# Performance work log

Measured on AMD Instinct MI355X. Metric: run time of the kernel, lower is better.

The kernel has to match this reference:

```python
import jax, jax.numpy as jnp
import numpy as np

N = 100000
IN_DIM, HID_DIM, EMB_DIM = 128, 64, 32
E = 1600000


def _gcn_conv(x, W, b, src, tgt, n):
    """PyG GCNConv: linear transform, add self-loops, sym-normalized scatter-add.
    W: [in, out], b: [out]. src/tgt: [E'] incl. self-loops handled by caller."""
    h = x @ W  # [n, out] -- transform before propagate (PyG order)
    deg = jax.ops.segment_sum(jnp.ones_like(tgt, dtype=h.dtype), tgt, num_segments=n)
    dinv = jnp.where(deg > 0, jax.lax.rsqrt(deg), 0.0)
    norm = dinv[src] * dinv[tgt]  # [E']
    msgs = h[src] * norm[:, None]  # [E', out]
    out = jax.ops.segment_sum(msgs, tgt, num_segments=n)
    return out + b


def setup_inputs() -> dict:
    key = jax.random.key(0)
    ks = jax.random.split(key, 6)
    x = jax.random.normal(ks[0], (N, IN_DIM), dtype=jnp.float32)
    edge_index = jax.random.randint(ks[1], (2, E), 0, N, dtype=jnp.int64)
    s1 = 1.0 / np.sqrt(IN_DIM)
    s2 = 1.0 / np.sqrt(HID_DIM)
    W1 = jax.random.uniform(ks[2], (IN_DIM, HID_DIM), jnp.float32, -s1, s1)
    b1 = jnp.zeros((HID_DIM,), jnp.float32)
    W2 = jax.random.uniform(ks[3], (HID_DIM, EMB_DIM), jnp.float32, -s2, s2)
    b2 = jnp.zeros((EMB_DIM,), jnp.float32)
    return {"x": x, "W1": W1, "b1": b1, "W2": W2, "b2": b2, "edge_index": edge_index}


def reference(x, W1, b1, W2, b2, edge_index):
    n = x.shape[0]
    src, tgt = edge_index[0], edge_index[1]
    # add self-loops once (same graph used by both convs)
    loops = jnp.arange(n, dtype=edge_index.dtype)
    src_sl = jnp.concatenate([src, loops])
    tgt_sl = jnp.concatenate([tgt, loops])
    h = jax.nn.relu(_gcn_conv(x, W1, b1, src_sl, tgt_sl, n))
    z = _gcn_conv(h, W2, b2, src_sl, tgt_sl, n)  # [n, EMB_DIM]
    # decode on original edges: edge-wise dot product
    recon = jnp.sum(z[src] * z[tgt], axis=1)  # [E]
    return z, recon
```

## Files before the change

kernel.cpp:

```cpp
#include <hip/hip_runtime.h>
#include <hip/hip_fp16.h>
#include <math.h>


#define NBMAX 256
#define BSHIFT 9
#define BNODES 512
#define CH 4096
#define CAPSHIFT 14
#define CAP (1 << CAPSHIFT)

typedef _Float16 half8 __attribute__((ext_vector_type(8)));
typedef float floatx4 __attribute__((ext_vector_type(4)));

static inline int divup(int a, int b) { return (a + b - 1) / b; }

__device__ inline void acc8(__half2* a, float4 v) {
    const __half2* h = (const __half2*)&v;
    a[0] = __hadd2(a[0], h[0]);
    a[1] = __hadd2(a[1], h[1]);
    a[2] = __hadd2(a[2], h[2]);
    a[3] = __hadd2(a[3], h[3]);
}
__device__ inline unsigned short f2bf(float f) {
    unsigned u = __builtin_bit_cast(unsigned, f);
    u = (u + 0x7FFFu + ((u >> 16) & 1u)) >> 16;
    return (unsigned short)u;
}


__global__ void k_init(int* __restrict__ gcur, unsigned* __restrict__ hs_pad,
                       unsigned* __restrict__ zs_pad) {
    int t = threadIdx.x;
    if (t < NBMAX) gcur[t] = t << CAPSHIFT;
    if (t < 32) hs_pad[t] = 0;
    else if (t < 48) zs_pad[t - 32] = 0;
}


__global__ __launch_bounds__(256) void k_part(const int* __restrict__ src,
                                              const int* __restrict__ tgt,
                                              int* __restrict__ gcur,
                                              unsigned* __restrict__ ebuf, int E, int NB) {
    __shared__ int h[NBMAX];
    __shared__ int base[NBMAX];
    int tid = threadIdx.x;
    int e0 = blockIdx.x * CH;
    for (int b = tid; b < NB; b += 256) h[b] = 0;
    __syncthreads();
    unsigned pk[CH / 256];
    int sv[CH / 256];
#pragma unroll
    for (int r = 0; r < CH / 256; r++) {
        int e = e0 + r * 256 + tid;
        if (e < E) {
            int t = tgt[e];
            int b = t >> BSHIFT;
            int l = atomicAdd(&h[b], 1);
            pk[r] = ((unsigned)b << 21) | ((unsigned)(t & (BNODES - 1)) << 12) | (unsigned)l;
            sv[r] = src[e];
        } else {
            pk[r] = 0xFFFFFFFFu;
        }
    }
    __syncthreads();
    for (int b = tid; b < NB; b += 256) {
        int c = h[b];
        base[b] = c ? atomicAdd(&gcur[b], c) : 0;
    }
    __syncthreads();
#pragma unroll
    for (int r = 0; r < CH / 256; r++) {
        if (pk[r] != 0xFFFFFFFFu) {
            int b = pk[r] >> 21;
            unsigned lt = (pk[r] >> 12) & (BNODES - 1);
            int l = pk[r] & 4095;
            ebuf[base[b] + l] = (lt << 23) | (unsigned)sv[r];
        }
    }
}


__global__ __launch_bounds__(512) void k_bfill(const unsigned* __restrict__ ebuf,
                                               const int* __restrict__ gcur,
                                               int* __restrict__ rowbeg,
                                               int* __restrict__ rowend,
                                               int* __restrict__ col,
                                               float* __restrict__ dinv, int n) {
    __shared__ int s_cnt[BNODES];
    __shared__ int s_scan[BNODES];
    __shared__ int s_cur[BNODES];
    int b = blockIdx.x, tid = threadIdx.x;
    int nbase = b << BSHIFT;
    int ebase = b << CAPSHIFT;
    int eend = gcur[b];
    s_cnt[tid] = 0;
    __syncthreads();
    for (int e = ebase + tid; e < eend; e += BNODES) {
        atomicAdd(&s_cnt[ebuf[e] >> 23], 1);
    }
    __syncthreads();
    s_scan[tid] = s_cnt[tid];
    __syncthreads();
    for (int off = 1; off < BNODES; off <<= 1) {
        int t = (tid >= off) ? s_scan[tid - off] : 0;
        __syncthreads();
        s_scan[tid] += t;
        __syncthreads();
    }
    int excl = s_scan[tid] - s_cnt[tid];
    s_cur[tid] = excl;
    int node = nbase + tid;
    if (node < n) {
        rowbeg[node] = ebase + excl;
        rowend[node] = ebase + excl + s_cnt[tid];
        dinv[node] = rsqrtf((float)(s_cnt[tid] + 1));
    }
    __syncthreads();
    for (int e = ebase + tid; e < eend; e += BNODES) {
        unsigned p = ebuf[e];
        int pos = atomicAdd(&s_cur[p >> 23], 1);
        col[ebase + pos] = (int)(p & 0x7FFFFFu);
    }
}


__global__ __launch_bounds__(256) void k_mm1(const float* __restrict__ x,
                                             const float* __restrict__ W1,
                                             const float* __restrict__ dinv,
                                             __half* __restrict__ hs, int n) {
    __shared__ _Float16 xh[64 * 136];
    __shared__ _Float16 Wt[64 * 136];
    int tid = threadIdx.x;
    int nbase = blockIdx.x * 64;
#pragma unroll
    for (int i = 0; i < 8; i++) {
        int f = tid + i * 256;
        int r = f >> 5, c4 = f & 31;
        int node = nbase + r;
        float4 v = make_float4(0.f, 0.f, 0.f, 0.f);
        if (node < n) v = *(const float4*)(x + (size_t)node * 128 + c4 * 4);
        union { uint2 u; __half2 h[2]; } pk;
        pk.h[0] = __floats2half2_rn(v.x, v.y);
        pk.h[1] = __floats2half2_rn(v.z, v.w);
        *(uint2*)&xh[r * 136 + c4 * 4] = pk.u;
    }
#pragma unroll
    for (int i = 0; i < 16; i++) {
        int f = tid + i * 256;
        int c = f & 63, kp = f >> 6;
        float a = W1[(size_t)(2 * kp) * 64 + c];
        float b = W1[(size_t)(2 * kp + 1) * 64 + c];
        *(__half2*)&Wt[c * 136 + 2 * kp] = __floats2half2_rn(a, b);
    }
    __syncthreads();
    int w = tid >> 6, lane = tid & 63;
    int quad = lane >> 4, m = lane & 15;
    floatx4 acc[4] = {{0.f, 0.f, 0.f, 0.f}, {0.f, 0.f, 0.f, 0.f},
                      {0.f, 0.f, 0.f, 0.f}, {0.f, 0.f, 0.f, 0.f}};
#pragma unroll
    for (int kt = 0; kt < 4; kt++) {
        half8 a = *(const half8*)&xh[(w * 16 + m) * 136 + kt * 32 + quad * 8];
#pragma unroll
        for (int ct = 0; ct < 4; ct++) {
            half8 b = *(const half8*)&Wt[(ct * 16 + m) * 136 + kt * 32 + quad * 8];
            acc[ct] = __builtin_amdgcn_mfma_f32_16x16x32_f16(a, b, acc[ct], 0, 0, 0);
        }
    }
#pragma unroll
    for (int reg = 0; reg < 4; reg++) {
        int node = nbase + w * 16 + quad * 4 + reg;
        if (node < n) {
            float d = dinv[node];
#pragma unroll
            for (int ct = 0; ct < 4; ct++) {
                hs[(size_t)node * 64 + ct * 16 + m] = __float2half(acc[ct][reg] * d);
            }
        }
    }
}


__global__ __launch_bounds__(256) void k_conv1(const __half* __restrict__ hs,
                                               const int* __restrict__ rowbeg,
                                               const int* __restrict__ rowend,
                                               const int* __restrict__ col,
                                               const float* __restrict__ dinv,
                                               const float* __restrict__ b1,
                                               __half* __restrict__ h2, int n) {
    int w = (blockIdx.x * 256 + threadIdx.x) >> 6;
    int lane = threadIdx.x & 63;
    if (w >= n) return;
    int el = lane >> 3, fl = lane & 7;
    int beg = rowbeg[w], end = rowend[w];
    int deg = end - beg;
    int m = min(64, deg);
    int sl = (lane < m) ? col[beg + lane] : 0;
    int s0 = __shfl(sl, el);
    int s1 = __shfl(sl, 8 + el);
    int s2 = __shfl(sl, 16 + el);
    int s3 = __shfl(sl, 24 + el);
    int r0 = (el < m) ? s0 : n;
    int r1 = (8 + el < m) ? s1 : n;
    int r2 = (16 + el < m) ? s2 : n;
    int r3 = (24 + el < m) ? s3 : n;
    int rs = (el == 0) ? w : n;
    float4 S = *(const float4*)(hs + (size_t)rs * 64 + fl * 8);
    float4 A = *(const float4*)(hs + (size_t)r0 * 64 + fl * 8);
    float4 B = *(const float4*)(hs + (size_t)r1 * 64 + fl * 8);
    float4 C = *(const float4*)(hs + (size_t)r2 * 64 + fl * 8);
    float4 D = *(const float4*)(hs + (size_t)r3 * 64 + fl * 8);
    __half2 a2[4];
#pragma unroll
    for (int j = 0; j < 4; j++) a2[j] = __half2half2(__float2half(0.f));
    acc8(a2, S);
    acc8(a2, A);
    acc8(a2, B);
    acc8(a2, C);
    acc8(a2, D);
    if (deg > 32) {
        for (int i = 32; i < m; i += 8) {
            int idx = i + el;
            int s = __shfl(sl, idx & 63);
            int a = (idx < m) ? s : n;
            float4 v = *(const float4*)(hs + (size_t)a * 64 + fl * 8);
            acc8(a2, v);
        }
        for (int e0 = beg + 64; e0 < end; e0 += 64) {
            int mc = min(64, end - e0);
            int sl2 = (lane < mc) ? col[e0 + lane] : 0;
            for (int i = 0; i < mc; i += 8) {
                int idx = i + el;
                int s = __shfl(sl2, idx & 63);
                int a = (idx < mc) ? s : n;
                float4 v = *(const float4*)(hs + (size_t)a * 64 + fl * 8);
                acc8(a2, v);
            }
        }
    }
    float r[8];
#pragma unroll
    for (int j = 0; j < 4; j++) {
        float2 f = __half22float2(a2[j]);
        r[2 * j] = f.x;
        r[2 * j + 1] = f.y;
    }
    for (int d = 8; d < 64; d <<= 1)
#pragma unroll
        for (int j = 0; j < 8; j++) r[j] += __shfl_xor(r[j], d);

    if (el == 0) {
        float d = dinv[w];
        float4 bb0 = *(const float4*)(b1 + fl * 8);
        float4 bb1 = *(const float4*)(b1 + fl * 8 + 4);
        union { float4 f; __half2 h[4]; } u;
        u.h[0] = __floats2half2_rn(fmaxf(r[0] * d + bb0.x, 0.f),
                                   fmaxf(r[1] * d + bb0.y, 0.f));
        u.h[1] = __floats2half2_rn(fmaxf(r[2] * d + bb0.z, 0.f),
                                   fmaxf(r[3] * d + bb0.w, 0.f));
        u.h[2] = __floats2half2_rn(fmaxf(r[4] * d + bb1.x, 0.f),
                                   fmaxf(r[5] * d + bb1.y, 0.f));
        u.h[3] = __floats2half2_rn(fmaxf(r[6] * d + bb1.z, 0.f),
                                   fmaxf(r[7] * d + bb1.w, 0.f));
        *(float4*)(h2 + (size_t)w * 64 + fl * 8) = u.f;
    }
}


__global__ __launch_bounds__(256) void k_mm2(const __half* __restrict__ h2,
                                             const float* __restrict__ W2,
                                             const float* __restrict__ dinv,
                                             __half* __restrict__ zs, int n) {
    __shared__ _Float16 Wt[32 * 72];
    int tid = threadIdx.x;
    int nbase = blockIdx.x * 64;
#pragma unroll
    for (int i = 0; i < 4; i++) {
        int f = tid + i * 256;
        int c = f & 31, kp = f >> 5;
        float a = W2[(size_t)(2 * kp) * 32 + c];
        float b = W2[(size_t)(2 * kp + 1) * 32 + c];
        *(__half2*)&Wt[c * 72 + 2 * kp] = __floats2half2_rn(a, b);
    }
    __syncthreads();
    int w = tid >> 6, lane = tid & 63;
    int quad = lane >> 4, m = lane & 15;
    int arow = nbase + w * 16 + m;
    const __half* abase = h2 + (size_t)min(arow, n - 1) * 64;
    floatx4 acc[2] = {{0.f, 0.f, 0.f, 0.f}, {0.f, 0.f, 0.f, 0.f}};
#pragma unroll
    for (int kt = 0; kt < 2; kt++) {
        half8 a = *(const half8*)(abase + kt * 32 + quad * 8);
#pragma unroll
        for (int ct = 0; ct < 2; ct++) {
            half8 b = *(const half8*)&Wt[(ct * 16 + m) * 72 + kt * 32 + quad * 8];
            acc[ct] = __builtin_amdgcn_mfma_f32_16x16x32_f16(a, b, acc[ct], 0, 0, 0);
        }
    }
#pragma unroll
    for (int reg = 0; reg < 4; reg++) {
        int node = nbase + w * 16 + quad * 4 + reg;
        if (node < n) {
            float d = dinv[node];
#pragma unroll
            for (int ct = 0; ct < 2; ct++) {
                zs[(size_t)node * 32 + ct * 16 + m] = __float2half(acc[ct][reg] * d);
            }
        }
    }
}


__global__ __launch_bounds__(256) void k_conv2(const __half* __restrict__ zs,
                                               const int* __restrict__ rowbeg,
                                               const int* __restrict__ rowend,
                                               const int* __restrict__ col,
                                               const float* __restrict__ dinv,
                                               const float* __restrict__ b2,
                                               float* __restrict__ zout,
                                               unsigned short* __restrict__ zh, int n) {
    int w = (blockIdx.x * 256 + threadIdx.x) >> 6;
    int lane = threadIdx.x & 63;
    if (w >= n) return;
    int el = lane >> 2, fl = lane & 3;
    int beg = rowbeg[w], end = rowend[w];
    int deg = end - beg;
    int m = min(64, deg);
    int sl = (lane < m) ? col[beg + lane] : 0;
    int s0 = __shfl(sl, el);
    int s1 = __shfl(sl, 16 + el);
    int r0 = (el < m) ? s0 : n;
    int r1 = (16 + el < m) ? s1 : n;
    int rs = (el == 0) ? w : n;
    float4 S = *(const float4*)(zs + (size_t)rs * 32 + fl * 8);
    float4 A = *(const float4*)(zs + (size_t)r0 * 32 + fl * 8);
    float4 B = *(const float4*)(zs + (size_t)r1 * 32 + fl * 8);
    __half2 a2[4];
#pragma unroll
    for (int j = 0; j < 4; j++) a2[j] = __half2half2(__float2half(0.f));
    acc8(a2, S);
    acc8(a2, A);
    acc8(a2, B);
    if (deg > 32) {
        int s2 = __shfl(sl, 32 + el);
        int s3 = __shfl(sl, 48 + el);
        int r2 = (32 + el < m) ? s2 : n;
        int r3 = (48 + el < m) ? s3 : n;
        float4 C = *(const float4*)(zs + (size_t)r2 * 32 + fl * 8);
        float4 D = *(const float4*)(zs + (size_t)r3 * 32 + fl * 8);
        acc8(a2, C);
        acc8(a2, D);
        for (int e0 = beg + 64; e0 < end; e0 += 64) {
            int mc = min(64, end - e0);
            int sl2 = (lane < mc) ? col[e0 + lane] : 0;
            for (int i = 0; i < mc; i += 16) {
                int idx = i + el;
                int s = __shfl(sl2, idx & 63);
                int a = (idx < mc) ? s : n;
                float4 v = *(const float4*)(zs + (size_t)a * 32 + fl * 8);
                acc8(a2, v);
            }
        }
    }
    float r[8];
#pragma unroll
    for (int j = 0; j < 4; j++) {
        float2 f = __half22float2(a2[j]);
        r[2 * j] = f.x;
        r[2 * j + 1] = f.y;
    }
    for (int d = 4; d < 64; d <<= 1)
#pragma unroll
        for (int j = 0; j < 8; j++) r[j] += __shfl_xor(r[j], d);

    if (el == 0) {
        float d = dinv[w];
        float4 bb0 = *(const float4*)(b2 + fl * 8);
        float4 bb1 = *(const float4*)(b2 + fl * 8 + 4);
        float o0 = r[0] * d + bb0.x, o1 = r[1] * d + bb0.y;
        float o2 = r[2] * d + bb0.z, o3 = r[3] * d + bb0.w;
        float o4 = r[4] * d + bb1.x, o5 = r[5] * d + bb1.y;
        float o6 = r[6] * d + bb1.z, o7 = r[7] * d + bb1.w;
        *(float4*)(zout + (size_t)w * 32 + fl * 8) = make_float4(o0, o1, o2, o3);
        *(float4*)(zout + (size_t)w * 32 + fl * 8 + 4) = make_float4(o4, o5, o6, o7);
        uint4 p;
        p.x = (unsigned)f2bf(o0) | ((unsigned)f2bf(o1) << 16);
        p.y = (unsigned)f2bf(o2) | ((unsigned)f2bf(o3) << 16);
        p.z = (unsigned)f2bf(o4) | ((unsigned)f2bf(o5) << 16);
        p.w = (unsigned)f2bf(o6) | ((unsigned)f2bf(o7) << 16);
        *(uint4*)(zh + (size_t)w * 32 + fl * 8) = p;
    }
}


__device__ inline float bfdot8(uint4 a, uint4 b) {
    const unsigned* pa = (const unsigned*)&a;
    const unsigned* pb = (const unsigned*)&b;
    float v = 0.f;
#pragma unroll
    for (int w = 0; w < 4; w++) {
        float alo = __builtin_bit_cast(float, pa[w] << 16);
        float ahi = __builtin_bit_cast(float, pa[w] & 0xFFFF0000u);
        float blo = __builtin_bit_cast(float, pb[w] << 16);
        float bhi = __builtin_bit_cast(float, pb[w] & 0xFFFF0000u);
        v += alo * blo + ahi * bhi;
    }
    return v;
}

__global__ __launch_bounds__(256) void k_decode(const unsigned short* __restrict__ zh,
                                                const int* __restrict__ src,
                                                const int* __restrict__ tgt,
                                                float* __restrict__ recon, int E) {
    int g = (blockIdx.x * 256 + threadIdx.x) >> 2;
    int fl = threadIdx.x & 3;
    int e0 = g * 4;
    if (e0 >= E) return;
    int cnt = min(4, E - e0);
    int s[4], t[4];
#pragma unroll
    for (int q = 0; q < 4; q++) {
        int e = (q < cnt) ? e0 + q : e0;
        s[q] = src[e];
        t[q] = tgt[e];
    }
    uint4 Za[4], Zb[4];
#pragma unroll
    for (int q = 0; q < 4; q++) {
        Za[q] = *(const uint4*)(zh + (size_t)s[q] * 32 + fl * 8);
        Zb[q] = *(const uint4*)(zh + (size_t)t[q] * 32 + fl * 8);
    }
    float v[4];
#pragma unroll
    for (int q = 0; q < 4; q++) {
        float x = bfdot8(Za[q], Zb[q]);
        x += __shfl_xor(x, 1);
        x += __shfl_xor(x, 2);
        v[q] = x;
    }
    if (fl == 0) {
        if (cnt == 4) {
            *(float4*)(recon + e0) = make_float4(v[0], v[1], v[2], v[3]);
        } else {
            for (int q = 0; q < cnt; q++) recon[e0 + q] = v[q];
        }
    }
}

extern "C" void kernel_launch(void* const* d_in, const int* in_sizes, int n_in,
                              void* d_out, int out_size, void* d_ws, size_t ws_size,
                              hipStream_t stream) {
    const float* x = (const float*)d_in[0];
    const float* W1 = (const float*)d_in[1];
    const float* b1 = (const float*)d_in[2];
    const float* W2 = (const float*)d_in[3];
    const float* b2 = (const float*)d_in[4];
    const int* ei = (const int*)d_in[5];

    int N = in_sizes[0] / 128;
    int E = in_sizes[5] / 2;
    const int* src = ei;
    const int* tgt = ei + E;
    int NB = divup(N, BNODES);

    char* ws = (char*)d_ws;
    size_t off = 0;
    auto alloc = [&](size_t bytes) {
        size_t r = off;
        off += (bytes + 255) & ~(size_t)255;
        return r;
    };
    int* gcur = (int*)(ws + alloc(NBMAX * 4));
    unsigned* ebuf = (unsigned*)(ws + alloc((size_t)NB * CAP * 4));
    int* col = (int*)(ws + alloc((size_t)NB * CAP * 4));
    int* rowbeg = (int*)(ws + alloc((size_t)N * 4));
    int* rowend = (int*)(ws + alloc((size_t)N * 4));
    float* dinv = (float*)(ws + alloc((size_t)N * 4));
    __half* hs = (__half*)(ws + alloc((size_t)(N + 1) * 64 * 2));
    __half* h2 = (__half*)(ws + alloc((size_t)N * 64 * 2));
    __half* zs = (__half*)(ws + alloc((size_t)(N + 1) * 32 * 2));
    unsigned short* zh = (unsigned short*)(ws + alloc((size_t)N * 32 * 2));

    float* zout = (float*)d_out;
    float* recon = zout + (size_t)N * 32;

    k_init<<<1, 256, 0, stream>>>(gcur, (unsigned*)(hs + (size_t)N * 64),
                                  (unsigned*)(zs + (size_t)N * 32));
    k_part<<<divup(E, CH), 256, 0, stream>>>(src, tgt, gcur, ebuf, E, NB);
    k_bfill<<<NB, BNODES, 0, stream>>>(ebuf, gcur, rowbeg, rowend, col, dinv, N);

    k_mm1<<<divup(N, 64), 256, 0, stream>>>(x, W1, dinv, hs, N);
    k_conv1<<<divup(N, 4), 256, 0, stream>>>(hs, rowbeg, rowend, col, dinv, b1, h2, N);
    k_mm2<<<divup(N, 64), 256, 0, stream>>>(h2, W2, dinv, zs, N);
    k_conv2<<<divup(N, 4), 256, 0, stream>>>(zs, rowbeg, rowend, col, dinv, b2, zout, zh, N);
    k_decode<<<divup(E, 256), 256, 0, stream>>>(zh, src, tgt, recon, E);
}
```

Before: 258.7 us.

## Process two nodes per wavefront in GCN aggregation kernels using half-wave groups

Both conv aggregation kernels now split each 64-lane wavefront into two 32-lane halves, each handling its own target node, and the grid is halved to match. Average in-degree is about 17, so a full wave per node left many lanes idle and paid per-row overhead once per wave; packing two rows per wave is meant to raise lane utilization and cut wave count. In exchange there is more divergence between the halves, whose degrees differ, and the reduction tree is shortened to stay within 32 lanes.

```diff
diff --git a/kernel.cpp b/kernel.cpp
--- a/kernel.cpp
+++ b/kernel.cpp
@@ -188,22 +188,25 @@
                                                const float* __restrict__ dinv,
                                                const float* __restrict__ b1,
                                                __half* __restrict__ h2, int n) {
-    int w = (blockIdx.x * 256 + threadIdx.x) >> 6;
+    int gw = (blockIdx.x * 256 + threadIdx.x) >> 6;
     int lane = threadIdx.x & 63;
+    int half = lane >> 5, ln = lane & 31;
+    int w = gw * 2 + half;
     if (w >= n) return;
-    int el = lane >> 3, fl = lane & 7;
+    int hbase = half << 5;
+    int el = ln >> 3, fl = ln & 7;
     int beg = rowbeg[w], end = rowend[w];
     int deg = end - beg;
-    int m = min(64, deg);
-    int sl = (lane < m) ? col[beg + lane] : 0;
-    int s0 = __shfl(sl, el);
-    int s1 = __shfl(sl, 8 + el);
-    int s2 = __shfl(sl, 16 + el);
-    int s3 = __shfl(sl, 24 + el);
+    int m = min(32, deg);
+    int sl = (ln < m) ? col[beg + ln] : 0;
+    int s0 = __shfl(sl, hbase + el);
+    int s1 = __shfl(sl, hbase + 4 + el);
+    int s2 = __shfl(sl, hbase + 8 + el);
+    int s3 = __shfl(sl, hbase + 12 + el);
     int r0 = (el < m) ? s0 : n;
-    int r1 = (8 + el < m) ? s1 : n;
-    int r2 = (16 + el < m) ? s2 : n;
-    int r3 = (24 + el < m) ? s3 : n;
+    int r1 = (4 + el < m) ? s1 : n;
+    int r2 = (8 + el < m) ? s2 : n;
+    int r3 = (12 + el < m) ? s3 : n;
     int rs = (el == 0) ? w : n;
     float4 S = *(const float4*)(hs + (size_t)rs * 64 + fl * 8);
     float4 A = *(const float4*)(hs + (size_t)r0 * 64 + fl * 8);
@@ -218,20 +221,31 @@
     acc8(a2, B);
     acc8(a2, C);
     acc8(a2, D);
+    if (deg > 16) {
+        int t0 = __shfl(sl, hbase + 16 + el);
+        int t1 = __shfl(sl, hbase + 20 + el);
+        int t2 = __shfl(sl, hbase + 24 + el);
+        int t3 = __shfl(sl, hbase + 28 + el);
+        int q0 = (16 + el < m) ? t0 : n;
+        int q1 = (20 + el < m) ? t1 : n;
+        int q2 = (24 + el < m) ? t2 : n;
+        int q3 = (28 + el < m) ? t3 : n;
+        float4 E0 = *(const float4*)(hs + (size_t)q0 * 64 + fl * 8);
+        float4 E1 = *(const float4*)(hs + (size_t)q1 * 64 + fl * 8);
+        float4 E2 = *(const float4*)(hs + (size_t)q2 * 64 + fl * 8);
+        float4 E3 = *(const float4*)(hs + (size_t)q3 * 64 + fl * 8);
+        acc8(a2, E0);
+        acc8(a2, E1);
+        acc8(a2, E2);
+        acc8(a2, E3);
+    }
     if (deg > 32) {
-        for (int i = 32; i < m; i += 8) {
-            int idx = i + el;
-            int s = __shfl(sl, idx & 63);
-            int a = (idx < m) ? s : n;
-            float4 v = *(const float4*)(hs + (size_t)a * 64 + fl * 8);
-            acc8(a2, v);
-        }
-        for (int e0 = beg + 64; e0 < end; e0 += 64) {
-            int mc = min(64, end - e0);
-            int sl2 = (lane < mc) ? col[e0 + lane] : 0;
-            for (int i = 0; i < mc; i += 8) {
+        for (int b0 = 32; b0 < deg; b0 += 32) {
+            int mc = min(32, deg - b0);
+            int sl2 = (ln < mc) ? col[beg + b0 + ln] : 0;
+            for (int i = 0; i < mc; i += 4) {
                 int idx = i + el;
-                int s = __shfl(sl2, idx & 63);
+                int s = __shfl(sl2, hbase + (idx & 31));
                 int a = (idx < mc) ? s : n;
                 float4 v = *(const float4*)(hs + (size_t)a * 64 + fl * 8);
                 acc8(a2, v);
@@ -245,7 +259,8 @@
         r[2 * j] = f.x;
         r[2 * j + 1] = f.y;
     }
-    for (int d = 8; d < 64; d <<= 1)
+#pragma unroll
+    for (int d = 8; d < 32; d <<= 1)
 #pragma unroll
         for (int j = 0; j < 8; j++) r[j] += __shfl_xor(r[j], d);
 
@@ -319,18 +334,21 @@
                                                const float* __restrict__ b2,
                                                float* __restrict__ zout,
                                                unsigned short* __restrict__ zh, int n) {
-    int w = (blockIdx.x * 256 + threadIdx.x) >> 6;
+    int gw = (blockIdx.x * 256 + threadIdx.x) >> 6;
     int lane = threadIdx.x & 63;
+    int half = lane >> 5, ln = lane & 31;
+    int w = gw * 2 + half;
     if (w >= n) return;
-    int el = lane >> 2, fl = lane & 3;
+    int hbase = half << 5;
+    int el = ln >> 2, fl = ln & 3;
     int beg = rowbeg[w], end = rowend[w];
     int deg = end - beg;
-    int m = min(64, deg);
-    int sl = (lane < m) ? col[beg + lane] : 0;
-    int s0 = __shfl(sl, el);
-    int s1 = __shfl(sl, 16 + el);
+    int m = min(32, deg);
+    int sl = (ln < m) ? col[beg + ln] : 0;
+    int s0 = __shfl(sl, hbase + el);
+    int s1 = __shfl(sl, hbase + 8 + el);
     int r0 = (el < m) ? s0 : n;
-    int r1 = (16 + el < m) ? s1 : n;
+    int r1 = (8 + el < m) ? s1 : n;
     int rs = (el == 0) ? w : n;
     float4 S = *(const float4*)(zs + (size_t)rs * 32 + fl * 8);
     float4 A = *(const float4*)(zs + (size_t)r0 * 32 + fl * 8);
@@ -341,21 +359,23 @@
     acc8(a2, S);
     acc8(a2, A);
     acc8(a2, B);
-    if (deg > 32) {
-        int s2 = __shfl(sl, 32 + el);
-        int s3 = __shfl(sl, 48 + el);
-        int r2 = (32 + el < m) ? s2 : n;
-        int r3 = (48 + el < m) ? s3 : n;
+    if (deg > 16) {
+        int s2 = __shfl(sl, hbase + 16 + el);
+        int s3 = __shfl(sl, hbase + 24 + el);
+        int r2 = (16 + el < m) ? s2 : n;
+        int r3 = (24 + el < m) ? s3 : n;
         float4 C = *(const float4*)(zs + (size_t)r2 * 32 + fl * 8);
         float4 D = *(const float4*)(zs + (size_t)r3 * 32 + fl * 8);
         acc8(a2, C);
         acc8(a2, D);
-        for (int e0 = beg + 64; e0 < end; e0 += 64) {
-            int mc = min(64, end - e0);
-            int sl2 = (lane < mc) ? col[e0 + lane] : 0;
-            for (int i = 0; i < mc; i += 16) {
+    }
+    if (deg > 32) {
+        for (int b0 = 32; b0 < deg; b0 += 32) {
+            int mc = min(32, deg - b0);
+            int sl2 = (ln < mc) ? col[beg + b0 + ln] : 0;
+            for (int i = 0; i < mc; i += 8) {
                 int idx = i + el;
-                int s = __shfl(sl2, idx & 63);
+                int s = __shfl(sl2, hbase + (idx & 31));
                 int a = (idx < mc) ? s : n;
                 float4 v = *(const float4*)(zs + (size_t)a * 32 + fl * 8);
                 acc8(a2, v);
@@ -369,7 +389,8 @@
         r[2 * j] = f.x;
         r[2 * j + 1] = f.y;
     }
-    for (int d = 4; d < 64; d <<= 1)
+#pragma unroll
+    for (int d = 4; d < 32; d <<= 1)
 #pragma unroll
         for (int j = 0; j < 8; j++) r[j] += __shfl_xor(r[j], d);
 
@@ -490,8 +511,8 @@
     k_bfill<<<NB, BNODES, 0, stream>>>(ebuf, gcur, rowbeg, rowend, col, dinv, N);
 
     k_mm1<<<divup(N, 64), 256, 0, stream>>>(x, W1, dinv, hs, N);
-    k_conv1<<<divup(N, 4), 256, 0, stream>>>(hs, rowbeg, rowend, col, dinv, b1, h2, N);
+    k_conv1<<<divup(N, 8), 256, 0, stream>>>(hs, rowbeg, rowend, col, dinv, b1, h2, N);
     k_mm2<<<divup(N, 64), 256, 0, stream>>>(h2, W2, dinv, zs, N);
-    k_conv2<<<divup(N, 4), 256, 0, stream>>>(zs, rowbeg, rowend, col, dinv, b2, zout, zh, N);
+    k_conv2<<<divup(N, 8), 256, 0, stream>>>(zs, rowbeg, rowend, col, dinv, b2, zout, zh, N);
     k_decode<<<divup(E, 256), 256, 0, stream>>>(zh, src, tgt, recon, E);
 }
```

New measurement: 233.8 us. 9.6% less time.

## Map four nodes per wavefront in GCN aggregation and vectorize edge partition loads

Applied to the files above, without the earlier changes.

The aggregation kernels now give each node a 16-lane quarter-wavefront instead of a full 64-lane wavefront, which cuts wasted lanes for the typical degree of about 17 and shrinks the cross-lane reduction. Neighbor indices are fetched in 16-wide chunks with unrolled batches of gathers, and the launch grid is reduced to match. The partition kernel reads src and tgt with int4 vector loads, giving each thread four consecutive edges. In exchange, high-degree nodes loop over more chunks per quarter-wave, and the per-lane edge order within each bucket changes.

```diff
diff --git a/kernel.cpp b/kernel.cpp
--- a/kernel.cpp
+++ b/kernel.cpp
@@ -48,19 +48,40 @@
     int e0 = blockIdx.x * CH;
     for (int b = tid; b < NB; b += 256) h[b] = 0;
     __syncthreads();
-    unsigned pk[CH / 256];
-    int sv[CH / 256];
-#pragma unroll
-    for (int r = 0; r < CH / 256; r++) {
-        int e = e0 + r * 256 + tid;
-        if (e < E) {
-            int t = tgt[e];
-            int b = t >> BSHIFT;
-            int l = atomicAdd(&h[b], 1);
-            pk[r] = ((unsigned)b << 21) | ((unsigned)(t & (BNODES - 1)) << 12) | (unsigned)l;
-            sv[r] = src[e];
+    unsigned pk[16];
+    int sv[16];
+#pragma unroll
+    for (int r = 0; r < 4; r++) {
+        int e = e0 + (r * 256 + tid) * 4;
+        if (e + 3 < E) {
+            int4 t4 = *(const int4*)(tgt + e);
+            int4 s4 = *(const int4*)(src + e);
+            int tv[4] = {t4.x, t4.y, t4.z, t4.w};
+            int sw[4] = {s4.x, s4.y, s4.z, s4.w};
+#pragma unroll
+            for (int j = 0; j < 4; j++) {
+                int t = tv[j];
+                int b = t >> BSHIFT;
+                int l = atomicAdd(&h[b], 1);
+                pk[r * 4 + j] = ((unsigned)b << 21) |
+                                ((unsigned)(t & (BNODES - 1)) << 12) | (unsigned)l;
+                sv[r * 4 + j] = sw[j];
+            }
         } else {
-            pk[r] = 0xFFFFFFFFu;
+#pragma unroll
+            for (int j = 0; j < 4; j++) {
+                int ee = e + j;
+                if (ee < E) {
+                    int t = tgt[ee];
+                    int b = t >> BSHIFT;
+                    int l = atomicAdd(&h[b], 1);
+                    pk[r * 4 + j] = ((unsigned)b << 21) |
+                                    ((unsigned)(t & (BNODES - 1)) << 12) | (unsigned)l;
+                    sv[r * 4 + j] = src[ee];
+                } else {
+                    pk[r * 4 + j] = 0xFFFFFFFFu;
+                }
+            }
         }
     }
     __syncthreads();
@@ -70,12 +91,12 @@
     }
     __syncthreads();
 #pragma unroll
-    for (int r = 0; r < CH / 256; r++) {
-        if (pk[r] != 0xFFFFFFFFu) {
-            int b = pk[r] >> 21;
-            unsigned lt = (pk[r] >> 12) & (BNODES - 1);
-            int l = pk[r] & 4095;
-            ebuf[base[b] + l] = (lt << 23) | (unsigned)sv[r];
+    for (int i = 0; i < 16; i++) {
+        if (pk[i] != 0xFFFFFFFFu) {
+            int b = pk[i] >> 21;
+            unsigned lt = (pk[i] >> 12) & (BNODES - 1);
+            int l = pk[i] & 4095;
+            ebuf[base[b] + l] = (lt << 23) | (unsigned)sv[i];
         }
     }
 }
@@ -188,50 +209,71 @@
                                                const float* __restrict__ dinv,
                                                const float* __restrict__ b1,
                                                __half* __restrict__ h2, int n) {
-    int w = (blockIdx.x * 256 + threadIdx.x) >> 6;
+    int gw = (blockIdx.x * 256 + threadIdx.x) >> 6;
     int lane = threadIdx.x & 63;
+    int q = lane >> 4, ln = lane & 15;
+    int w = gw * 4 + q;
     if (w >= n) return;
-    int el = lane >> 3, fl = lane & 7;
+    int qb = q << 4;
+    int el = ln >> 3, fl = ln & 7;
     int beg = rowbeg[w], end = rowend[w];
     int deg = end - beg;
-    int m = min(64, deg);
-    int sl = (lane < m) ? col[beg + lane] : 0;
-    int s0 = __shfl(sl, el);
-    int s1 = __shfl(sl, 8 + el);
-    int s2 = __shfl(sl, 16 + el);
-    int s3 = __shfl(sl, 24 + el);
-    int r0 = (el < m) ? s0 : n;
-    int r1 = (8 + el < m) ? s1 : n;
-    int r2 = (16 + el < m) ? s2 : n;
-    int r3 = (24 + el < m) ? s3 : n;
+    int m = min(16, deg);
+    int m2 = min(16, deg - 16);
+    int sl = (ln < m) ? col[beg + ln] : 0;
+    int sl2 = (ln < m2) ? col[beg + 16 + ln] : 0;
+    __half2 a2[4];
+#pragma unroll
+    for (int j = 0; j < 4; j++) a2[j] = __half2half2(__float2half(0.f));
     int rs = (el == 0) ? w : n;
     float4 S = *(const float4*)(hs + (size_t)rs * 64 + fl * 8);
-    float4 A = *(const float4*)(hs + (size_t)r0 * 64 + fl * 8);
-    float4 B = *(const float4*)(hs + (size_t)r1 * 64 + fl * 8);
-    float4 C = *(const float4*)(hs + (size_t)r2 * 64 + fl * 8);
-    float4 D = *(const float4*)(hs + (size_t)r3 * 64 + fl * 8);
-    __half2 a2[4];
-#pragma unroll
-    for (int j = 0; j < 4; j++) a2[j] = __half2half2(__float2half(0.f));
+    float4 L[4];
+#pragma unroll
+    for (int r = 0; r < 4; r++) {
+        int idx = 2 * r + el;
+        int s = __shfl(sl, qb + idx);
+        int a = (idx < m) ? s : n;
+        L[r] = *(const float4*)(hs + (size_t)a * 64 + fl * 8);
+    }
     acc8(a2, S);
-    acc8(a2, A);
-    acc8(a2, B);
-    acc8(a2, C);
-    acc8(a2, D);
+#pragma unroll
+    for (int r = 0; r < 4; r++) acc8(a2, L[r]);
+#pragma unroll
+    for (int r = 0; r < 4; r++) {
+        int idx = 8 + 2 * r + el;
+        int s = __shfl(sl, qb + idx);
+        int a = (idx < m) ? s : n;
+        L[r] = *(const float4*)(hs + (size_t)a * 64 + fl * 8);
+    }
+#pragma unroll
+    for (int r = 0; r < 4; r++) acc8(a2, L[r]);
+    if (deg > 16) {
+#pragma unroll
+        for (int r = 0; r < 4; r++) {
+            int idx = 2 * r + el;
+            int s = __shfl(sl2, qb + idx);
+            int a = (idx < m2) ? s : n;
+            L[r] = *(const float4*)(hs + (size_t)a * 64 + fl * 8);
+        }
+#pragma unroll
+        for (int r = 0; r < 4; r++) acc8(a2, L[r]);
+#pragma unroll
+        for (int r = 0; r < 4; r++) {
+            int idx = 8 + 2 * r + el;
+            int s = __shfl(sl2, qb + idx);
+            int a = (idx < m2) ? s : n;
+            L[r] = *(const float4*)(hs + (size_t)a * 64 + fl * 8);
+        }
+#pragma unroll
+        for (int r = 0; r < 4; r++) acc8(a2, L[r]);
+    }
     if (deg > 32) {
-        for (int i = 32; i < m; i += 8) {
-            int idx = i + el;
-            int s = __shfl(sl, idx & 63);
-            int a = (idx < m) ? s : n;
-            float4 v = *(const float4*)(hs + (size_t)a * 64 + fl * 8);
-            acc8(a2, v);
-        }
-        for (int e0 = beg + 64; e0 < end; e0 += 64) {
-            int mc = min(64, end - e0);
-            int sl2 = (lane < mc) ? col[e0 + lane] : 0;
-            for (int i = 0; i < mc; i += 8) {
-                int idx = i + el;
-                int s = __shfl(sl2, idx & 63);
+        for (int b0 = 32; b0 < deg; b0 += 16) {
+            int mc = min(16, deg - b0);
+            int sl3 = (ln < mc) ? col[beg + b0 + ln] : 0;
+            for (int r = 0; r < 8; r++) {
+                int idx = 2 * r + el;
+                int s = __shfl(sl3, qb + idx);
                 int a = (idx < mc) ? s : n;
                 float4 v = *(const float4*)(hs + (size_t)a * 64 + fl * 8);
                 acc8(a2, v);
@@ -245,9 +287,8 @@
         r[2 * j] = f.x;
         r[2 * j + 1] = f.y;
     }
-    for (int d = 8; d < 64; d <<= 1)
-#pragma unroll
-        for (int j = 0; j < 8; j++) r[j] += __shfl_xor(r[j], d);
+#pragma unroll
+    for (int j = 0; j < 8; j++) r[j] += __shfl_xor(r[j], 8);
 
     if (el == 0) {
         float d = dinv[w];
@@ -319,43 +360,53 @@
                                                const float* __restrict__ b2,
                                                float* __restrict__ zout,
                                                unsigned short* __restrict__ zh, int n) {
-    int w = (blockIdx.x * 256 + threadIdx.x) >> 6;
+    int gw = (blockIdx.x * 256 + threadIdx.x) >> 6;
     int lane = threadIdx.x & 63;
+    int q = lane >> 4, ln = lane & 15;
+    int w = gw * 4 + q;
     if (w >= n) return;
-    int el = lane >> 2, fl = lane & 3;
+    int qb = q << 4;
+    int el = ln >> 2, fl = ln & 3;
     int beg = rowbeg[w], end = rowend[w];
     int deg = end - beg;
-    int m = min(64, deg);
-    int sl = (lane < m) ? col[beg + lane] : 0;
-    int s0 = __shfl(sl, el);
-    int s1 = __shfl(sl, 16 + el);
-    int r0 = (el < m) ? s0 : n;
-    int r1 = (16 + el < m) ? s1 : n;
+    int m = min(16, deg);
+    int m2 = min(16, deg - 16);
+    int sl = (ln < m) ? col[beg + ln] : 0;
+    int sl2 = (ln < m2) ? col[beg + 16 + ln] : 0;
+    __half2 a2[4];
+#pragma unroll
+    for (int j = 0; j < 4; j++) a2[j] = __half2half2(__float2half(0.f));
     int rs = (el == 0) ? w : n;
     float4 S = *(const float4*)(zs + (size_t)rs * 32 + fl * 8);
-    float4 A = *(const float4*)(zs + (size_t)r0 * 32 + fl * 8);
-    float4 B = *(const float4*)(zs + (size_t)r1 * 32 + fl * 8);
-    __half2 a2[4];
-#pragma unroll
-    for (int j = 0; j < 4; j++) a2[j] = __half2half2(__float2half(0.f));
+    float4 L[4];
+#pragma unroll
+    for (int r = 0; r < 4; r++) {
+        int idx = 4 * r + el;
+        int s = __shfl(sl, qb + idx);
+        int a = (idx < m) ? s : n;
+        L[r] = *(const float4*)(zs + (size_t)a * 32 + fl * 8);
+    }
     acc8(a2, S);
-    acc8(a2, A);
-    acc8(a2, B);
+#pragma unroll
+    for (int r = 0; r < 4; r++) acc8(a2, L[r]);
+    if (deg > 16) {
+#pragma unroll
+        for (int r = 0; r < 4; r++) {
+            int idx = 4 * r + el;
+            int s = __shfl(sl2, qb + idx);
+            int a = (idx < m2) ? s : n;
+            L[r] = *(const float4*)(zs + (size_t)a * 32 + fl * 8);
+        }
+#pragma unroll
+        for (int r = 0; r < 4; r++) acc8(a2, L[r]);
+    }
     if (deg > 32) {
-        int s2 = __shfl(sl, 32 + el);
-        int s3 = __shfl(sl, 48 + el);
-        int r2 = (32 + el < m) ? s2 : n;
-        int r3 = (48 + el < m) ? s3 : n;
-        float4 C = *(const float4*)(zs + (size_t)r2 * 32 + fl * 8);
-        float4 D = *(const float4*)(zs + (size_t)r3 * 32 + fl * 8);
-        acc8(a2, C);
-        acc8(a2, D);
-        for (int e0 = beg + 64; e0 < end; e0 += 64) {
-            int mc = min(64, end - e0);
-            int sl2 = (lane < mc) ? col[e0 + lane] : 0;
-            for (int i = 0; i < mc; i += 16) {
-                int idx = i + el;
-                int s = __shfl(sl2, idx & 63);
+        for (int b0 = 32; b0 < deg; b0 += 16) {
+            int mc = min(16, deg - b0);
+            int sl3 = (ln < mc) ? col[beg + b0 + ln] : 0;
+            for (int r = 0; r < 4; r++) {
+                int idx = 4 * r + el;
+                int s = __shfl(sl3, qb + idx);
                 int a = (idx < mc) ? s : n;
                 float4 v = *(const float4*)(zs + (size_t)a * 32 + fl * 8);
                 acc8(a2, v);
@@ -369,7 +420,8 @@
         r[2 * j] = f.x;
         r[2 * j + 1] = f.y;
     }
-    for (int d = 4; d < 64; d <<= 1)
+#pragma unroll
+    for (int d = 4; d < 16; d <<= 1)
 #pragma unroll
         for (int j = 0; j < 8; j++) r[j] += __shfl_xor(r[j], d);
 
@@ -490,8 +542,8 @@
     k_bfill<<<NB, BNODES, 0, stream>>>(ebuf, gcur, rowbeg, rowend, col, dinv, N);
 
     k_mm1<<<divup(N, 64), 256, 0, stream>>>(x, W1, dinv, hs, N);
-    k_conv1<<<divup(N, 4), 256, 0, stream>>>(hs, rowbeg, rowend, col, dinv, b1, h2, N);
+    k_conv1<<<divup(N, 16), 256, 0, stream>>>(hs, rowbeg, rowend, col, dinv, b1, h2, N);
     k_mm2<<<divup(N, 64), 256, 0, stream>>>(h2, W2, dinv, zs, N);
-    k_conv2<<<divup(N, 4), 256, 0, stream>>>(zs, rowbeg, rowend, col, dinv, b2, zout, zh, N);
+    k_conv2<<<divup(N, 16), 256, 0, stream>>>(zs, rowbeg, rowend, col, dinv, b2, zout, zh, N);
     k_decode<<<divup(E, 256), 256, 0, stream>>>(zh, src, tgt, recon, E);
 }
```

Result: faster. 228.2 us (-11.8%).
